# Kernel optimization log

Measured on AMD Instinct MI355X. Metric: run time of the kernel, lower is better.

## Reference

```python
import jax, jax.numpy as jnp
import numpy as np

FIELDS, NUM, CAT = 39, 13, 26
D, M, V, B, DEEP = 16, 16, 100000, 4096, 400
LEFT, RIGHT = np.triu_indices(FIELDS, k=1)  # pair indices, Q = 741
Q = LEFT.size
EPS = 1e-5


def setup_inputs() -> dict:
    key = jax.random.key(0)
    ks = jax.random.split(key, 18)
    xi = jax.random.randint(ks[0], (B, CAT), 0, V)
    xv = jax.random.uniform(ks[1], (B, NUM), dtype=jnp.float32)
    # 2nd-order embedding tables, stacked since all fields share vocab size
    emb_tables = jax.random.normal(ks[2], (FIELDS, V, D), dtype=jnp.float32) * 0.1
    T3 = jax.random.normal(ks[3], (D, M, D), dtype=jnp.float32) * 0.05
    T2 = jax.random.normal(ks[4], (M, D * D), dtype=jnp.float32) * 0.05
    gc = jax.random.normal(ks[5], (Q,), dtype=jnp.float32)
    fi_w = jax.random.normal(ks[6], (Q * M, DEEP), dtype=jnp.float32) * 0.01
    fi_b = jnp.zeros((DEEP,), dtype=jnp.float32)
    fi_gamma = jnp.ones((DEEP,), dtype=jnp.float32)
    fi_beta = jnp.zeros((DEEP,), dtype=jnp.float32)
    emb_w = jax.random.normal(ks[7], (FIELDS * D, DEEP), dtype=jnp.float32) * 0.02
    emb_b = jnp.zeros((DEEP,), dtype=jnp.float32)
    emb_gamma = jnp.ones((DEEP,), dtype=jnp.float32)
    emb_beta = jnp.zeros((DEEP,), dtype=jnp.float32)
    fc_w = jax.random.normal(ks[8], (2 * DEEP, 1), dtype=jnp.float32) * 0.05
    fc_b = jnp.zeros((1,), dtype=jnp.float32)
    return {"xi": xi, "xv": xv, "emb_tables": emb_tables, "T3": T3, "T2": T2,
            "gc": gc, "fi_w": fi_w, "fi_b": fi_b, "fi_gamma": fi_gamma, "fi_beta": fi_beta,
            "emb_w": emb_w, "emb_b": emb_b, "emb_gamma": emb_gamma, "emb_beta": emb_beta,
            "fc_w": fc_w, "fc_b": fc_b}


def _bn(x, gamma, beta):
    # BatchNorm1d in training mode: batch statistics, biased variance
    mean = jnp.mean(x, axis=0)
    var = jnp.var(x, axis=0)
    return gamma * (x - mean) * jax.lax.rsqrt(var + EPS) + beta


def reference(xi, xv, emb_tables, T3, T2, gc, fi_w, fi_b, fi_gamma, fi_beta,
              emb_w, emb_b, emb_gamma, emb_beta, fc_w, fc_b):
    # numerical fields: embedding row 0 scaled by the raw value
    num_part = xv[:, :, None] * emb_tables[:NUM, 0, :][None]          # [B, 13, D]
    # categorical fields: per-field gather
    cat_part = emb_tables[NUM + jnp.arange(CAT)[None, :], xi]          # [B, 26, D]
    fm2 = jnp.concatenate([num_part, cat_part], axis=1)               # [B, 39, D]
    vi = fm2[:, LEFT]                                                  # [B, Q, D]
    vj = fm2[:, RIGHT]                                                 # [B, Q, D]
    # einsum('bqd,dmd,bqd->bm'): repeated d on T3 takes its diagonal -> [D, M]
    T3diag = jnp.einsum('dmd->dm', T3)
    ga = jnp.einsum('bqd,bqd,dm->bm', vi, vj, T3diag)                  # [B, M]
    ga = jax.nn.softmax(ga, axis=1)
    # T1 = einsum('bm,mn->bmn'); s = einsum('bqd,bmn,bqd->bqm') sums T1 over n
    t1_rowsum = ga * jnp.sum(T2, axis=1)[None, :]                      # [B, M]
    pair_dot = jnp.einsum('bqd,bqd->bq', vi, vj)                       # [B, Q]
    s = pair_dot[:, :, None] * t1_rowsum[:, None, :]                   # [B, Q, M]
    sh = (s * gc[None, :, None]).reshape(-1, Q * M)                    # [B, Q*M]
    th = jax.nn.relu(_bn(sh @ fi_w + fi_b, fi_gamma, fi_beta))         # [B, DEEP]
    emb = fm2.reshape(-1, FIELDS * D)                                  # [B, 39*D]
    emb = jax.nn.relu(_bn(emb @ emb_w + emb_b, emb_gamma, emb_beta))   # [B, DEEP]
    out = jnp.concatenate([th, emb], axis=1) @ fc_w + fc_b             # [B, 1]
    return jnp.sum(jax.nn.sigmoid(out), axis=1)                        # [B]
```

## Files before the change

### kernel.cpp

```cpp
#include <hip/hip_runtime.h>
#include <hip/hip_bf16.h>

#define BATCH 4096
#define FIELDS_ 39
#define NUMF 13
#define CATF 26
#define DD 16
#define MM 16
#define VV 100000
#define DEEP_ 400
#define QQ 741
#define QPAD 768
#define KE 624
#define KEP 640
#define NEP 512
#define N1 6400
#define NKTE 20
#define NT_ 24
#define EPS_ 1e-5f

#define OFF_ABF 0
#define OFF_T   (BATCH*QPAD/2)
#define OFF_W2  (OFF_T + BATCH*MM)
#define OFF_WE  (OFF_W2 + N1*QPAD/2)
#define OFF_FMB (OFF_WE + NEP*KEP/2)
#define OFF_TH  (OFF_FMB + BATCH*KEP/2)
#define OFF_EMB (OFF_TH + BATCH*DEEP_)
#define OFF_ACC (OFF_EMB + BATCH*DEEP_)
#define OFF_T2S (OFF_ACC + 1600)
#define OFF_T3D (OFF_T2S + 16)

typedef __attribute__((ext_vector_type(8))) short bf16x8;
typedef __attribute__((ext_vector_type(4))) float f32x4;

__device__ __forceinline__ ushort f2bf(float v) {
    union { float f; unsigned u; } x; x.f = v;
    unsigned r = x.u + 0x7fff + ((x.u >> 16) & 1);
    return (ushort)(r >> 16);
}
__device__ __forceinline__ unsigned pack2(float a, float b) {
    return (unsigned)f2bf(a) | ((unsigned)f2bf(b) << 16);
}
__device__ __forceinline__ void async16(void* lds, const void* g) {
    __builtin_amdgcn_global_load_lds(
        (const __attribute__((address_space(1))) unsigned int*)g,
        (__attribute__((address_space(3))) unsigned int*)lds,
        16, 0, 0);
}

__global__ __launch_bounds__(256) void kprep0(const float* __restrict__ T3,
                                              const float* __restrict__ T2,
                                              float* __restrict__ ws) {
    int tid = threadIdx.x;
    if (tid < MM) {
        float s = 0.f;
        for (int j = 0; j < DD * DD; ++j) s += T2[tid * DD * DD + j];
        ws[OFF_T2S + tid] = s;
    }
    if (tid < DD * MM) {
        int d = tid >> 4, m = tid & 15;
        ws[OFF_T3D + tid] = T3[(d * MM + m) * DD + d];
    }
    for (int i = tid; i < 1600; i += 256) ws[OFF_ACC + i] = 0.f;
}

__global__ __launch_bounds__(256) void kbig(const int* __restrict__ xi,
                                            const float* __restrict__ xv,
                                            const float* __restrict__ emb,
                                            const float* __restrict__ gc,
                                            const float* __restrict__ fi_w,
                                            const float* __restrict__ emb_w,
                                            float* __restrict__ ws,
                                            ushort* __restrict__ Abf,
                                            ushort* __restrict__ FMB,
                                            ushort* __restrict__ W2,
                                            ushort* __restrict__ WE) {
    __shared__ float smem[4200];
    int bid = blockIdx.x, tid = threadIdx.x;

    if (bid < BATCH) {
        float* row = smem;
        float* hsh = smem + 624;
        float* gash = smem + 640;
        ushort* stA = (ushort*)(smem + 656);
        ushort* stF = stA + QPAD;
        int b = bid;
        for (int e = tid; e < KE; e += 256) {
            int f = e >> 4, d = e & 15;
            float v;
            if (f < NUMF) {
                v = xv[b * NUMF + f] * emb[(long)f * VV * DD + d];
            } else {
                int c = f - NUMF;
                int idxv = xi[b * CATF + c];
                v = emb[((long)(NUMF + c) * VV + idxv) * DD + d];
            }
            row[e] = v;
        }
        __syncthreads();
        for (int e = tid; e < KEP; e += 256)
            stF[e] = (e < KE) ? f2bf(row[e]) : (ushort)0;
        if (tid < DD) {
            float s = 0.f, s2 = 0.f;
            for (int f = 0; f < FIELDS_; ++f) { float v = row[f * DD + tid]; s += v; s2 += v * v; }
            hsh[tid] = 0.5f * (s * s - s2);
        }
        __syncthreads();
        if (tid < MM) {
            float g = 0.f;
            for (int d = 0; d < DD; ++d) g += hsh[d] * ws[OFF_T3D + d * MM + tid];
            gash[tid] = g;
        }
        __syncthreads();
        if (tid < MM) {
            float mx = -1e30f;
            for (int m = 0; m < MM; ++m) mx = fmaxf(mx, gash[m]);
            float se = 0.f;
            for (int m = 0; m < MM; ++m) se += expf(gash[m] - mx);
            ws[OFF_T + b * MM + tid] = expf(gash[tid] - mx) / se * ws[OFF_T2S + tid];
        }
        for (int q = tid; q < QPAD; q += 256) {
            float av = 0.f;
            if (q < QQ) {
                int i = 0, qq = q, cnt = FIELDS_ - 1;
                while (qq >= cnt) { qq -= cnt; ++i; cnt = FIELDS_ - 1 - i; }
                int j = i + 1 + qq;
                float dot = 0.f;
#pragma unroll
                for (int d = 0; d < DD; ++d) dot += row[i * DD + d] * row[j * DD + d];
                av = dot * gc[q];
            }
            stA[q] = f2bf(av);
        }
        __syncthreads();
        if (tid < 96)
            *(uint4*)&Abf[(long)b * QPAD + tid * 8] = *(uint4*)&stA[tid * 8];
        else if (tid < 176)
            *(uint4*)&FMB[(long)b * KEP + (tid - 96) * 8] = *(uint4*)&stF[(tid - 96) * 8];
    } else if (bid < BATCH + 1536) {
        int bt = bid - BATCH;
        int kt = bt >> 6, m = (bt >> 2) & 15, ch = bt & 3;
        float* tile = smem;
        for (int i = tid; i < 32 * 25; i += 256) {
            int ql = i / 25, c4 = i - ql * 25;
            int q = kt * 32 + ql;
            float4 v = make_float4(0.f, 0.f, 0.f, 0.f);
            if (q < QQ) v = *(const float4*)&fi_w[(q * MM + m) * DEEP_ + ch * 100 + c4 * 4];
            tile[ql * 101 + c4 * 4 + 0] = v.x; tile[ql * 101 + c4 * 4 + 1] = v.y;
            tile[ql * 101 + c4 * 4 + 2] = v.z; tile[ql * 101 + c4 * 4 + 3] = v.w;
        }
        __syncthreads();
        for (int i = tid; i < 100 * 4; i += 256) {
            int lc = i >> 2, cq = i & 3;
            int kcol = ch * 100 + lc;
            unsigned r[4];
#pragma unroll
            for (int j = 0; j < 4; ++j)
                r[j] = pack2(tile[(cq * 8 + 2 * j) * 101 + lc], tile[(cq * 8 + 2 * j + 1) * 101 + lc]);
            *(uint4*)&W2[(long)(kcol * 16 + m) * QPAD + kt * 32 + cq * 8] =
                make_uint4(r[0], r[1], r[2], r[3]);
        }
    } else {
        int bt = bid - BATCH - 1536;
        int kt = bt >> 2, ch = bt & 3;
        float* tile = smem;
        for (int i = tid; i < 32 * 32; i += 256) {
            int kl = i >> 5, c4 = i & 31;
            int k = kt * 32 + kl;
            int n = ch * 128 + c4 * 4;
            float4 v = make_float4(0.f, 0.f, 0.f, 0.f);
            if (k < KE && n < DEEP_) v = *(const float4*)&emb_w[k * DEEP_ + n];
            tile[kl * 129 + c4 * 4 + 0] = v.x; tile[kl * 129 + c4 * 4 + 1] = v.y;
            tile[kl * 129 + c4 * 4 + 2] = v.z; tile[kl * 129 + c4 * 4 + 3] = v.w;
        }
        __syncthreads();
        for (int i = tid; i < 128 * 4; i += 256) {
            int nl = i >> 2, cq = i & 3;
            int n = ch * 128 + nl;
            uint4 o = make_uint4(0, 0, 0, 0);
            if (n < DEEP_) {
                unsigned r[4];
#pragma unroll
                for (int j = 0; j < 4; ++j)
                    r[j] = pack2(tile[(cq * 8 + 2 * j) * 129 + nl], tile[(cq * 8 + 2 * j + 1) * 129 + nl]);
                o = make_uint4(r[0], r[1], r[2], r[3]);
            }
            if (n < NEP)
                *(uint4*)&WE[(long)n * KEP + kt * 32 + cq * 8] = o;
        }
    }
}

__device__ __forceinline__ void pipeline3(const ushort* As, const ushort* Bs0,
                                          const ushort* Bs1, ushort* lds,
                                          int tid, int nt, int f1b, int f2b, int sw,
                                          f32x4 (*acc)[4]) {
#define STAGEP(SL, T) { \
    ushort* L_ = lds + (SL) * 12288; \
    async16(L_ + tid * 8, As + (T) * 32); \
    async16(L_ + 4096 + tid * 8, Bs0 + (T) * 32); \
    async16(L_ + 8192 + tid * 8, Bs1 + (T) * 32); }
    STAGEP(0, 0); STAGEP(1, 1);
    asm volatile("s_waitcnt vmcnt(3)" ::: "memory");
    __builtin_amdgcn_s_barrier();
    int sl = 0;
    for (int t = 0; t < nt; ++t) {
        __builtin_amdgcn_sched_barrier(0);
        const ushort* cur = lds + sl * 12288;
        bf16x8 f1[4], f2[4];
#pragma unroll
        for (int r = 0; r < 4; ++r) f1[r] = *(const bf16x8*)&cur[f1b + r * 512 + sw];
#pragma unroll
        for (int c = 0; c < 4; ++c) f2[c] = *(const bf16x8*)&cur[f2b + c * 512 + sw];
        int sl2 = sl + 2; if (sl2 >= 3) sl2 -= 3;
        if (t + 2 < nt) STAGEP(sl2, t + 2);
        __builtin_amdgcn_s_setprio(1);
#pragma unroll
        for (int r = 0; r < 4; ++r)
#pragma unroll
            for (int c = 0; c < 4; ++c)
                acc[r][c] = __builtin_amdgcn_mfma_f32_16x16x32_bf16(f1[r], f2[c], acc[r][c], 0, 0, 0);
        __builtin_amdgcn_s_setprio(0);
        if (t + 1 < nt) {
            if (t + 2 < nt) { asm volatile("s_waitcnt vmcnt(3)" ::: "memory"); }
            else            { asm volatile("s_waitcnt vmcnt(0)" ::: "memory"); }
            __builtin_amdgcn_s_barrier();
        }
        sl = sl + 1; if (sl >= 3) sl -= 3;
    }
#undef STAGEP
}

__global__ __launch_bounds__(512, 4) void kgemms(const ushort* __restrict__ Abf,
                                                 const ushort* __restrict__ W2,
                                                 const ushort* __restrict__ FMB,
                                                 const ushort* __restrict__ WE,
                                                 const float* __restrict__ Tmat,
                                                 float* __restrict__ TH,
                                                 float* __restrict__ EMB,
                                                 float* __restrict__ ACC) {
    __shared__ ushort ldsbuf[3 * 12288];
    __shared__ float red[512];
    int tid = threadIdx.x;
    int lane = tid & 63, wid = tid >> 6;
    int wb = wid >> 2, wn = wid & 3;
    int kq = lane >> 4, lr = lane & 15;
    int arow = tid >> 2, ac = tid & 3;
    int csw = (ac ^ ((arow >> 1) & 3)) * 8;
    int sw = (kq ^ ((lr >> 1) & 3)) * 8;
    red[tid] = 0.f;
    f32x4 acc[4][4] = {};
    int wg = blockIdx.x;

    if (wg < 800) {
        int s = (wg & 7) * 100 + (wg >> 3);
        int n0 = (s >> 5) * 256, b0 = (s & 31) * 128;
        const ushort* As  = Abf + (long)(b0 + arow) * QPAD + csw;
        const ushort* Bs0 = W2 + (long)(n0 + arow) * QPAD + csw;
        const ushort* Bs1 = W2 + (long)(n0 + 128 + arow) * QPAD + csw;
        pipeline3(As, Bs0, Bs1, ldsbuf, tid, NT_,
                  4096 + (wn * 64 + lr) * 32, (wb * 64 + lr) * 32, sw, acc);
        float* tbuf = (float*)ldsbuf;
        float ls[4] = {0.f, 0.f, 0.f, 0.f}, ls2[4] = {0.f, 0.f, 0.f, 0.f};
#pragma unroll
        for (int cg = 0; cg < 4; ++cg) {
            int bloc = wb * 64 + cg * 16 + lr;
            float4 t4 = *(const float4*)&Tmat[(b0 + bloc) * 16 + kq * 4];
#pragma unroll
            for (int r = 0; r < 4; ++r) {
                float v = acc[r][cg][0] * t4.x + acc[r][cg][1] * t4.y +
                          acc[r][cg][2] * t4.z + acc[r][cg][3] * t4.w;
                v += __shfl_xor(v, 16);
                v += __shfl_xor(v, 32);
                ls[r] += v; ls2[r] += v * v;
                if (kq == r) tbuf[bloc * 17 + wn * 4 + r] = v;
            }
        }
#pragma unroll
        for (int r = 0; r < 4; ++r) {
            float a = ls[r], b2 = ls2[r];
            a += __shfl_xor(a, 8, 16); b2 += __shfl_xor(b2, 8, 16);
            a += __shfl_xor(a, 4, 16); b2 += __shfl_xor(b2, 4, 16);
            a += __shfl_xor(a, 2, 16); b2 += __shfl_xor(b2, 2, 16);
            a += __shfl_xor(a, 1, 16); b2 += __shfl_xor(b2, 1, 16);
            if (lane == 0) {
                atomicAdd(&red[wn * 4 + r], a);
                atomicAdd(&red[16 + wn * 4 + r], b2);
            }
        }
        __syncthreads();
        if (tid < 16) {
            atomicAdd(&ACC[(n0 >> 4) + tid], red[tid]);
            atomicAdd(&ACC[800 + (n0 >> 4) + tid], red[16 + tid]);
        }
        {
            int rowl = tid >> 2, qf = tid & 3;
            float o0 = tbuf[rowl * 17 + qf * 4 + 0];
            float o1 = tbuf[rowl * 17 + qf * 4 + 1];
            float o2 = tbuf[rowl * 17 + qf * 4 + 2];
            float o3 = tbuf[rowl * 17 + qf * 4 + 3];
            *(float4*)&TH[(b0 + rowl) * DEEP_ + (n0 >> 4) + qf * 4] =
                make_float4(o0, o1, o2, o3);
        }
    } else {
        int e = wg - 800;
        int se = (e & 7) * 8 + (e >> 3);
        int n0 = (se >> 5) * 256, b0 = (se & 31) * 128;
        const ushort* As  = FMB + (long)(b0 + arow) * KEP + csw;
        const ushort* Bs0 = WE + (long)(n0 + arow) * KEP + csw;
        const ushort* Bs1 = WE + (long)(n0 + 128 + arow) * KEP + csw;
        pipeline3(As, Bs0, Bs1, ldsbuf, tid, NKTE,
                  (wb * 64 + lr) * 32, 4096 + (wn * 64 + lr) * 32, sw, acc);
#pragma unroll
        for (int cg = 0; cg < 4; ++cg) {
            int ncl = wn * 64 + cg * 16 + lr;
            int nc = n0 + ncl;
            float ls = 0.f, ls2 = 0.f;
#pragma unroll
            for (int r = 0; r < 4; ++r) {
#pragma unroll
                for (int j = 0; j < 4; ++j) {
                    float v = acc[r][cg][j];
                    int brow = b0 + wb * 64 + r * 16 + kq * 4 + j;
                    if (nc < DEEP_) EMB[brow * DEEP_ + nc] = v;
                    ls += v; ls2 += v * v;
                }
            }
            ls += __shfl_xor(ls, 16);  ls += __shfl_xor(ls, 32);
            ls2 += __shfl_xor(ls2, 16); ls2 += __shfl_xor(ls2, 32);
            if (lane < 16 && nc < DEEP_) {
                atomicAdd(&red[ncl], ls);
                atomicAdd(&red[256 + ncl], ls2);
            }
        }
        __syncthreads();
        if (tid < 256) {
            int nc = n0 + tid;
            if (nc < DEEP_) {
                atomicAdd(&ACC[400 + nc], red[tid]);
                atomicAdd(&ACC[1200 + nc], red[256 + tid]);
            }
        }
    }
}

__global__ __launch_bounds__(256) void kfinal(const float* __restrict__ fig,
                                              const float* __restrict__ fibeta,
                                              const float* __restrict__ eg,
                                              const float* __restrict__ ebeta,
                                              const float* __restrict__ fcw,
                                              const float* __restrict__ fcb,
                                              const float* __restrict__ ws,
                                              float* __restrict__ out) {
    int b = blockIdx.x, tid = threadIdx.x;
    float part = 0.f;
    if (tid < 200) {
        int c = tid * 4;
        int loc = (c < DEEP_) ? c : c - DEEP_;
        const float* xp = (c < DEEP_) ? &ws[OFF_TH + b * DEEP_ + loc]
                                      : &ws[OFF_EMB + b * DEEP_ + loc];
        float4 x = *(const float4*)xp;
        float4 g = *(const float4*)((c < DEEP_) ? &fig[loc] : &eg[loc]);
        float4 be = *(const float4*)((c < DEEP_) ? &fibeta[loc] : &ebeta[loc]);
        float4 sm = *(const float4*)&ws[OFF_ACC + c];
        float4 sq = *(const float4*)&ws[OFF_ACC + 800 + c];
        float4 w = *(const float4*)&fcw[c];
        const float* xv_ = (const float*)&x; const float* gv = (const float*)&g;
        const float* bev = (const float*)&be; const float* smv = (const float*)&sm;
        const float* sqv = (const float*)&sq; const float* wv = (const float*)&w;
#pragma unroll
        for (int j = 0; j < 4; ++j) {
            float mean = smv[j] * (1.f / BATCH);
            float var = sqv[j] * (1.f / BATCH) - mean * mean;
            float rstd = rsqrtf(var + EPS_);
            float v = fmaxf(gv[j] * (xv_[j] - mean) * rstd + bev[j], 0.f);
            part += v * wv[j];
        }
    }
    __shared__ float red[4];
#pragma unroll
    for (int off = 32; off > 0; off >>= 1) part += __shfl_down(part, off, 64);
    if ((tid & 63) == 0) red[tid >> 6] = part;
    __syncthreads();
    if (tid == 0) {
        float tot = red[0] + red[1] + red[2] + red[3] + fcb[0];
        out[b] = 1.f / (1.f + expf(-tot));
    }
}

extern "C" void kernel_launch(void* const* d_in, const int* in_sizes, int n_in,
                              void* d_out, int out_size, void* d_ws, size_t ws_size,
                              hipStream_t stream) {
    const int*   xi    = (const int*)d_in[0];
    const float* xv    = (const float*)d_in[1];
    const float* emb   = (const float*)d_in[2];
    const float* T3    = (const float*)d_in[3];
    const float* T2    = (const float*)d_in[4];
    const float* gc    = (const float*)d_in[5];
    const float* fi_w  = (const float*)d_in[6];
    const float* fig   = (const float*)d_in[8];
    const float* fibt  = (const float*)d_in[9];
    const float* emb_w = (const float*)d_in[10];
    const float* eg    = (const float*)d_in[12];
    const float* ebt   = (const float*)d_in[13];
    const float* fcw   = (const float*)d_in[14];
    const float* fcb   = (const float*)d_in[15];
    float* ws = (float*)d_ws;
    ushort* Abf = (ushort*)(ws + OFF_ABF);
    ushort* W2  = (ushort*)(ws + OFF_W2);
    ushort* WE  = (ushort*)(ws + OFF_WE);
    ushort* FMB = (ushort*)(ws + OFF_FMB);
    float* out = (float*)d_out;

    hipLaunchKernelGGL(kprep0, dim3(1), dim3(256), 0, stream, T3, T2, ws);
    hipLaunchKernelGGL(kbig, dim3(BATCH + 1536 + 80), dim3(256), 0, stream,
                       xi, xv, emb, gc, fi_w, emb_w, ws, Abf, FMB, W2, WE);
    hipLaunchKernelGGL(kgemms, dim3(864), dim3(512), 0, stream,
                       Abf, W2, FMB, WE, ws + OFF_T, ws + OFF_TH, ws + OFF_EMB, ws + OFF_ACC);
    hipLaunchKernelGGL(kfinal, dim3(BATCH), dim3(256), 0, stream,
                       fig, fibt, eg, ebt, fcw, fcb, ws, out);
}
```

Measured before the change: 91.49 us.

## Enlarge GEMM block tiles to 256x256 with 8x4 MFMA accumulators per wave

Both GEMMs in kgemms now use 256x256 output tiles instead of 128x256. Each wave computes 128x64 with an 8x4 accumulator array, and the grid is halved to 432 blocks. The three-stage LDS pipeline now stages four operand slabs per step. The aim is more operand reuse per byte loaded and half the global traffic per output, at the cost of more registers and LDS (occupancy bound lowered to 2) and fewer blocks to fill the CUs.

```diff
diff --git a/kernel.cpp b/kernel.cpp
--- a/kernel.cpp
+++ b/kernel.cpp
@@ -191,38 +191,40 @@
     }
 }
 
-__device__ __forceinline__ void pipeline3(const ushort* As, const ushort* Bs0,
-                                          const ushort* Bs1, ushort* lds,
-                                          int tid, int nt, int f1b, int f2b, int sw,
+__device__ __forceinline__ void pipeline3(const ushort* p0, const ushort* p1,
+                                          const ushort* p2, const ushort* p3,
+                                          ushort* lds, int tid, int nt,
+                                          int f1b, int f2b, int sw,
                                           f32x4 (*acc)[4]) {
 #define STAGEP(SL, T) { \
-    ushort* L_ = lds + (SL) * 12288; \
-    async16(L_ + tid * 8, As + (T) * 32); \
-    async16(L_ + 4096 + tid * 8, Bs0 + (T) * 32); \
-    async16(L_ + 8192 + tid * 8, Bs1 + (T) * 32); }
+    ushort* L_ = lds + (SL) * 16384; \
+    async16(L_ + tid * 8,         p0 + (T) * 32); \
+    async16(L_ + 4096 + tid * 8,  p1 + (T) * 32); \
+    async16(L_ + 8192 + tid * 8,  p2 + (T) * 32); \
+    async16(L_ + 12288 + tid * 8, p3 + (T) * 32); }
     STAGEP(0, 0); STAGEP(1, 1);
-    asm volatile("s_waitcnt vmcnt(3)" ::: "memory");
+    asm volatile("s_waitcnt vmcnt(4)" ::: "memory");
     __builtin_amdgcn_s_barrier();
     int sl = 0;
     for (int t = 0; t < nt; ++t) {
         __builtin_amdgcn_sched_barrier(0);
-        const ushort* cur = lds + sl * 12288;
-        bf16x8 f1[4], f2[4];
-#pragma unroll
-        for (int r = 0; r < 4; ++r) f1[r] = *(const bf16x8*)&cur[f1b + r * 512 + sw];
+        const ushort* cur = lds + sl * 16384;
+        bf16x8 f1[8], f2[4];
+#pragma unroll
+        for (int r = 0; r < 8; ++r) f1[r] = *(const bf16x8*)&cur[f1b + r * 512 + sw];
 #pragma unroll
         for (int c = 0; c < 4; ++c) f2[c] = *(const bf16x8*)&cur[f2b + c * 512 + sw];
         int sl2 = sl + 2; if (sl2 >= 3) sl2 -= 3;
         if (t + 2 < nt) STAGEP(sl2, t + 2);
         __builtin_amdgcn_s_setprio(1);
 #pragma unroll
-        for (int r = 0; r < 4; ++r)
+        for (int r = 0; r < 8; ++r)
 #pragma unroll
             for (int c = 0; c < 4; ++c)
                 acc[r][c] = __builtin_amdgcn_mfma_f32_16x16x32_bf16(f1[r], f2[c], acc[r][c], 0, 0, 0);
         __builtin_amdgcn_s_setprio(0);
         if (t + 1 < nt) {
-            if (t + 2 < nt) { asm volatile("s_waitcnt vmcnt(3)" ::: "memory"); }
+            if (t + 2 < nt) { asm volatile("s_waitcnt vmcnt(4)" ::: "memory"); }
             else            { asm volatile("s_waitcnt vmcnt(0)" ::: "memory"); }
             __builtin_amdgcn_s_barrier();
         }
@@ -231,7 +233,7 @@
 #undef STAGEP
 }
 
-__global__ __launch_bounds__(512, 4) void kgemms(const ushort* __restrict__ Abf,
+__global__ __launch_bounds__(512, 2) void kgemms(const ushort* __restrict__ Abf,
                                                  const ushort* __restrict__ W2,
                                                  const ushort* __restrict__ FMB,
                                                  const ushort* __restrict__ WE,
@@ -239,53 +241,56 @@
                                                  float* __restrict__ TH,
                                                  float* __restrict__ EMB,
                                                  float* __restrict__ ACC) {
-    __shared__ ushort ldsbuf[3 * 12288];
+    __shared__ ushort ldsbuf[3 * 16384];
     __shared__ float red[512];
     int tid = threadIdx.x;
     int lane = tid & 63, wid = tid >> 6;
-    int wb = wid >> 2, wn = wid & 3;
+    int wB = wid >> 2;
+    int wS = wid & 3;
     int kq = lane >> 4, lr = lane & 15;
-    int arow = tid >> 2, ac = tid & 3;
-    int csw = (ac ^ ((arow >> 1) & 3)) * 8;
+    int rr = tid >> 2, ac = tid & 3;
+    int csw = (ac ^ ((rr >> 1) & 3)) * 8;
     int sw = (kq ^ ((lr >> 1) & 3)) * 8;
     red[tid] = 0.f;
-    f32x4 acc[4][4] = {};
+    f32x4 acc[8][4] = {};
     int wg = blockIdx.x;
 
-    if (wg < 800) {
-        int s = (wg & 7) * 100 + (wg >> 3);
-        int n0 = (s >> 5) * 256, b0 = (s & 31) * 128;
-        const ushort* As  = Abf + (long)(b0 + arow) * QPAD + csw;
-        const ushort* Bs0 = W2 + (long)(n0 + arow) * QPAD + csw;
-        const ushort* Bs1 = W2 + (long)(n0 + 128 + arow) * QPAD + csw;
-        pipeline3(As, Bs0, Bs1, ldsbuf, tid, NT_,
-                  4096 + (wn * 64 + lr) * 32, (wb * 64 + lr) * 32, sw, acc);
+    if (wg < 400) {
+        int s = (wg & 7) * 50 + (wg >> 3);
+        int b0 = (s / 25) * 256;
+        int n0 = (s % 25) * 256;
+        const ushort* p0 = Abf + (long)(b0 + rr) * QPAD + csw;
+        const ushort* p1 = Abf + (long)(b0 + 128 + rr) * QPAD + csw;
+        const ushort* p2 = W2 + (long)(n0 + rr) * QPAD + csw;
+        const ushort* p3 = W2 + (long)(n0 + 128 + rr) * QPAD + csw;
+        pipeline3(p0, p1, p2, p3, ldsbuf, tid, NT_,
+                  8192 + (wB * 128 + lr) * 32, (wS * 64 + lr) * 32, sw, acc);
         float* tbuf = (float*)ldsbuf;
-        float ls[4] = {0.f, 0.f, 0.f, 0.f}, ls2[4] = {0.f, 0.f, 0.f, 0.f};
+        float ls[8] = {}, ls2[8] = {};
 #pragma unroll
         for (int cg = 0; cg < 4; ++cg) {
-            int bloc = wb * 64 + cg * 16 + lr;
+            int bloc = wS * 64 + cg * 16 + lr;
             float4 t4 = *(const float4*)&Tmat[(b0 + bloc) * 16 + kq * 4];
 #pragma unroll
-            for (int r = 0; r < 4; ++r) {
+            for (int r = 0; r < 8; ++r) {
                 float v = acc[r][cg][0] * t4.x + acc[r][cg][1] * t4.y +
                           acc[r][cg][2] * t4.z + acc[r][cg][3] * t4.w;
                 v += __shfl_xor(v, 16);
                 v += __shfl_xor(v, 32);
                 ls[r] += v; ls2[r] += v * v;
-                if (kq == r) tbuf[bloc * 17 + wn * 4 + r] = v;
-            }
-        }
-#pragma unroll
-        for (int r = 0; r < 4; ++r) {
+                if (lane < 16) tbuf[bloc * 17 + wB * 8 + r] = v;
+            }
+        }
+#pragma unroll
+        for (int r = 0; r < 8; ++r) {
             float a = ls[r], b2 = ls2[r];
             a += __shfl_xor(a, 8, 16); b2 += __shfl_xor(b2, 8, 16);
             a += __shfl_xor(a, 4, 16); b2 += __shfl_xor(b2, 4, 16);
             a += __shfl_xor(a, 2, 16); b2 += __shfl_xor(b2, 2, 16);
             a += __shfl_xor(a, 1, 16); b2 += __shfl_xor(b2, 1, 16);
             if (lane == 0) {
-                atomicAdd(&red[wn * 4 + r], a);
-                atomicAdd(&red[16 + wn * 4 + r], b2);
+                atomicAdd(&red[wB * 8 + r], a);
+                atomicAdd(&red[16 + wB * 8 + r], b2);
             }
         }
         __syncthreads();
@@ -294,34 +299,41 @@
             atomicAdd(&ACC[800 + (n0 >> 4) + tid], red[16 + tid]);
         }
         {
-            int rowl = tid >> 2, qf = tid & 3;
-            float o0 = tbuf[rowl * 17 + qf * 4 + 0];
-            float o1 = tbuf[rowl * 17 + qf * 4 + 1];
-            float o2 = tbuf[rowl * 17 + qf * 4 + 2];
-            float o3 = tbuf[rowl * 17 + qf * 4 + 3];
-            *(float4*)&TH[(b0 + rowl) * DEEP_ + (n0 >> 4) + qf * 4] =
-                make_float4(o0, o1, o2, o3);
+            int rowl = tid >> 1, kcb = (tid & 1) * 8;
+            float o0 = tbuf[rowl * 17 + kcb + 0];
+            float o1 = tbuf[rowl * 17 + kcb + 1];
+            float o2 = tbuf[rowl * 17 + kcb + 2];
+            float o3 = tbuf[rowl * 17 + kcb + 3];
+            float o4 = tbuf[rowl * 17 + kcb + 4];
+            float o5 = tbuf[rowl * 17 + kcb + 5];
+            float o6 = tbuf[rowl * 17 + kcb + 6];
+            float o7 = tbuf[rowl * 17 + kcb + 7];
+            float* dst = &TH[(b0 + rowl) * DEEP_ + (n0 >> 4) + kcb];
+            *(float4*)dst = make_float4(o0, o1, o2, o3);
+            *(float4*)(dst + 4) = make_float4(o4, o5, o6, o7);
         }
     } else {
-        int e = wg - 800;
-        int se = (e & 7) * 8 + (e >> 3);
-        int n0 = (se >> 5) * 256, b0 = (se & 31) * 128;
-        const ushort* As  = FMB + (long)(b0 + arow) * KEP + csw;
-        const ushort* Bs0 = WE + (long)(n0 + arow) * KEP + csw;
-        const ushort* Bs1 = WE + (long)(n0 + 128 + arow) * KEP + csw;
-        pipeline3(As, Bs0, Bs1, ldsbuf, tid, NKTE,
-                  (wb * 64 + lr) * 32, 4096 + (wn * 64 + lr) * 32, sw, acc);
+        int e = wg - 400;
+        int se = (e & 7) * 4 + (e >> 3);
+        int b0 = (se >> 1) * 256;
+        int n0 = (se & 1) * 256;
+        const ushort* p0 = FMB + (long)(b0 + rr) * KEP + csw;
+        const ushort* p1 = FMB + (long)(b0 + 128 + rr) * KEP + csw;
+        const ushort* p2 = WE + (long)(n0 + rr) * KEP + csw;
+        const ushort* p3 = WE + (long)(n0 + 128 + rr) * KEP + csw;
+        pipeline3(p0, p1, p2, p3, ldsbuf, tid, NKTE,
+                  (wB * 128 + lr) * 32, 8192 + (wS * 64 + lr) * 32, sw, acc);
 #pragma unroll
         for (int cg = 0; cg < 4; ++cg) {
-            int ncl = wn * 64 + cg * 16 + lr;
+            int ncl = wS * 64 + cg * 16 + lr;
             int nc = n0 + ncl;
             float ls = 0.f, ls2 = 0.f;
 #pragma unroll
-            for (int r = 0; r < 4; ++r) {
+            for (int r = 0; r < 8; ++r) {
 #pragma unroll
                 for (int j = 0; j < 4; ++j) {
                     float v = acc[r][cg][j];
-                    int brow = b0 + wb * 64 + r * 16 + kq * 4 + j;
+                    int brow = b0 + wB * 128 + r * 16 + kq * 4 + j;
                     if (nc < DEEP_) EMB[brow * DEEP_ + nc] = v;
                     ls += v; ls2 += v * v;
                 }
@@ -415,7 +427,7 @@
     hipLaunchKernelGGL(kprep0, dim3(1), dim3(256), 0, stream, T3, T2, ws);
     hipLaunchKernelGGL(kbig, dim3(BATCH + 1536 + 80), dim3(256), 0, stream,
                        xi, xv, emb, gc, fi_w, emb_w, ws, Abf, FMB, W2, WE);
-    hipLaunchKernelGGL(kgemms, dim3(864), dim3(512), 0, stream,
+    hipLaunchKernelGGL(kgemms, dim3(432), dim3(512), 0, stream,
                        Abf, W2, FMB, WE, ws + OFF_T, ws + OFF_TH, ws + OFF_EMB, ws + OFF_ACC);
     hipLaunchKernelGGL(kfinal, dim3(BATCH), dim3(256), 0, stream,
                        fig, fibt, eg, ebt, fcw, fcb, ws, out);
```

Result: faster. 89.47 us (-2.2%).
